# Kernel tuning notes

Measured on AMD Instinct MI355X. Metric: run time of the kernel, lower is better.

Reference implementation:

```python
import jax, jax.numpy as jnp
import numpy as np

NUM_HEADS = 8


def setup_inputs() -> dict:
    key = jax.random.key(0)
    ks = jax.random.split(key, 8)
    b, m, d = 8, 2048, 512
    sc = 1.0 / np.sqrt(d)
    return {
        "x": jax.random.normal(ks[0], (b, m, d), jnp.float32),
        "w_q": jax.random.normal(ks[1], (d, d), jnp.float32) * sc,
        "w_k": jax.random.normal(ks[2], (d, d), jnp.float32) * sc,
        "w_v": jax.random.normal(ks[3], (d, d), jnp.float32) * sc,
        "in_proj_w": jax.random.normal(ks[4], (3 * d, d), jnp.float32) * sc,
        "in_proj_b": jax.random.normal(ks[5], (3 * d,), jnp.float32) * 0.01,
        "out_w": jax.random.normal(ks[6], (d, d), jnp.float32) * sc,
        "out_b": jax.random.normal(ks[7], (d,), jnp.float32) * 0.01,
    }


def _rope_cos_sin(m, d):
    # faithful to source: theta = 10000 ** (-2*(i-1)/d), i = 0..d/2-1
    i = jnp.arange(d // 2, dtype=jnp.float32)
    theta = jnp.power(10000.0, -2.0 * (i - 1.0) / d)
    ang = jnp.arange(m, dtype=jnp.float32)[:, None] * theta  # [m, d/2]
    return jnp.cos(ang), jnp.sin(ang)


def reference(x, w_q, w_k, w_v, in_proj_w, in_proj_b, out_w, out_b):
    b, m, d = x.shape
    h, hd = NUM_HEADS, d // NUM_HEADS
    c, s = _rope_cos_sin(m, d)

    def rot(t):
        # equivalent to t[pos] @ R[pos] with the source's block-rotation matrix
        te = t.reshape(b, m, d // 2, 2)
        e, o = te[..., 0], te[..., 1]
        return jnp.stack([e * c + o * s, -e * s + o * c], axis=-1).reshape(b, m, d)

    q = rot(x @ w_q.T)
    k = rot(x @ w_k.T)
    v = rot(x @ w_v.T)

    # nn.MultiheadAttention's internal in_proj
    wqi, wki, wvi = jnp.split(in_proj_w, 3, axis=0)
    bqi, bki, bvi = jnp.split(in_proj_b, 3, axis=0)
    q = (q @ wqi.T + bqi).reshape(b, m, h, hd)
    k = (k @ wki.T + bki).reshape(b, m, h, hd)
    v = (v @ wvi.T + bvi).reshape(b, m, h, hd)

    scale = 1.0 / jnp.sqrt(jnp.asarray(hd, x.dtype))
    scores = jnp.einsum("bqhd,bkhd->bhqk", q, k) * scale
    causal = jnp.triu(jnp.ones((m, m), bool), k=1)
    scores = jnp.where(causal, jnp.finfo(x.dtype).min, scores)
    attn = jax.nn.softmax(scores, axis=-1)
    ctx = jnp.einsum("bhqk,bkhd->bqhd", attn, v).reshape(b, m, d)
    return ctx @ out_w.T + out_b
```

## Files before the change

kernel.cpp:

```cpp
#include <hip/hip_runtime.h>
#include <hip/hip_bf16.h>

typedef __attribute__((ext_vector_type(8))) short short8;
typedef __attribute__((ext_vector_type(4))) short short4v;
typedef __attribute__((ext_vector_type(4))) float f32x4;

__device__ __forceinline__ float bf2f(unsigned short u) {
    union { unsigned int i; float f; } v; v.i = ((unsigned int)u) << 16; return v.f;
}
__device__ __forceinline__ unsigned short f2bfh(float f) {
    union { __hip_bfloat16 h; unsigned short u; } c;
    c.h = __float2bfloat16(f);
    return c.u;
}

#define GLDS16(g, l) __builtin_amdgcn_global_load_lds( \
    (const __attribute__((address_space(1))) unsigned int*)(g), \
    (__attribute__((address_space(3))) unsigned int*)(l), 16, 0, 0)

__global__ __launch_bounds__(256) void cvt_one(
    const float* __restrict__ in, unsigned short* __restrict__ out, int nchunk)
{
    int i = blockIdx.x * 256 + threadIdx.x;
    if (i >= nchunk) return;
    f32x4 a = *(const f32x4*)&in[(size_t)i * 8];
    f32x4 b = *(const f32x4*)&in[(size_t)i * 8 + 4];
    short8 o;
    o[0] = (short)f2bfh(a[0]); o[1] = (short)f2bfh(a[1]);
    o[2] = (short)f2bfh(a[2]); o[3] = (short)f2bfh(a[3]);
    o[4] = (short)f2bfh(b[0]); o[5] = (short)f2bfh(b[1]);
    o[6] = (short)f2bfh(b[2]); o[7] = (short)f2bfh(b[3]);
    *(short8*)&out[(size_t)i * 8] = o;
}

__global__ __launch_bounds__(256) void cvt_w(
    const float* __restrict__ wq, const float* __restrict__ wk, const float* __restrict__ wv,
    const float* __restrict__ ipw, const float* __restrict__ ow,
    unsigned short* __restrict__ wqb, unsigned short* __restrict__ ipwb,
    unsigned short* __restrict__ owb)
{
    int z = blockIdx.y;
    const float* src;
    unsigned short* dst;
    if (z < 3)      { src = (z == 0 ? wq : z == 1 ? wk : wv); dst = wqb + (size_t)z * 262144; }
    else if (z < 6) { src = ipw + (size_t)(z - 3) * 262144;   dst = ipwb + (size_t)(z - 3) * 262144; }
    else            { src = ow;                                dst = owb; }
    int i = blockIdx.x * 256 + threadIdx.x;
    f32x4 a = *(const f32x4*)&src[(size_t)i * 8];
    f32x4 b = *(const f32x4*)&src[(size_t)i * 8 + 4];
    short8 o;
    o[0] = (short)f2bfh(a[0]); o[1] = (short)f2bfh(a[1]);
    o[2] = (short)f2bfh(a[2]); o[3] = (short)f2bfh(a[3]);
    o[4] = (short)f2bfh(b[0]); o[5] = (short)f2bfh(b[1]);
    o[6] = (short)f2bfh(b[2]); o[7] = (short)f2bfh(b[3]);
    *(short8*)&dst[(size_t)i * 8] = o;
}

__global__ __launch_bounds__(256) void rope_table(float* __restrict__ ct, float* __restrict__ st)
{
    int i = threadIdx.x;
    int pos = blockIdx.x;
    const float THC = -0.05190512648261308f;
    float theta = exp2f(THC * ((float)i - 1.0f));
    float ang = (float)pos * theta;
    float sn, cs;
    sincosf(ang, &sn, &cs);
    ct[pos * 256 + i] = cs;
    st[pos * 256 + i] = sn;
}

__device__ __forceinline__ void gemm_core(
    const unsigned short* __restrict__ A, int lda,
    const unsigned short* __restrict__ B, int K,
    int rowBase, int colBase, int tid, int lane, int wave,
    short* As, short* Bs, f32x4 (&acc)[4][4])
{
    const int wr = wave >> 1, wc = wave & 1;
    const int lo = lane & 15, hi = lane >> 4;
    for (int k0 = 0; k0 < K; k0 += 64) {
        const unsigned short* Ab = A + (size_t)rowBase * lda + k0;
        const unsigned short* Bb = B + (size_t)colBase * K + k0;
        #pragma unroll
        for (int p = 0; p < 4; ++p) {
            int o = p * 256 + tid;
            GLDS16(&Ab[(size_t)(o >> 3) * lda + (o & 7) * 8], &As[o * 8]);
        }
        #pragma unroll
        for (int p = 0; p < 4; ++p) {
            int o = p * 256 + tid;
            GLDS16(&Bb[(size_t)(o >> 3) * K + (o & 7) * 8], &Bs[o * 8]);
        }
        __syncthreads();
        #pragma unroll
        for (int s = 0; s < 2; ++s) {
            short8 a[4], b[4];
            #pragma unroll
            for (int i = 0; i < 4; ++i)
                a[i] = *(const short8*)&As[(wr * 64 + i * 16 + lo) * 64 + s * 32 + hi * 8];
            #pragma unroll
            for (int j = 0; j < 4; ++j)
                b[j] = *(const short8*)&Bs[(wc * 64 + j * 16 + lo) * 64 + s * 32 + hi * 8];
            #pragma unroll
            for (int i = 0; i < 4; ++i)
                #pragma unroll
                for (int j = 0; j < 4; ++j)
                    acc[i][j] = __builtin_amdgcn_mfma_f32_16x16x32_bf16(a[i], b[j], acc[i][j], 0, 0, 0);
        }
        __syncthreads();
    }
}

template<int HAS_BIAS, int OUT>
__global__ __launch_bounds__(256) void gemm_bt(
    const unsigned short* __restrict__ A, int lda, const unsigned short* __restrict__ B,
    const float* __restrict__ bias, void* __restrict__ Cp,
    int M, int N, int K)
{
    __shared__ __align__(16) short As[128 * 64];
    __shared__ __align__(16) short Bs[128 * 64];
    const int tid = threadIdx.x, lane = tid & 63, wave = tid >> 6;
    const int wr = wave >> 1, wc = wave & 1;
    const int lo = lane & 15, hi = lane >> 4;
    const int rowBase = blockIdx.y * 128;
    const int colBase = blockIdx.x * 128;

    f32x4 acc[4][4] = {};
    gemm_core(A, lda, B, K, rowBase, colBase, tid, lane, wave, As, Bs, acc);

    #pragma unroll
    for (int i = 0; i < 4; ++i) {
        int rowA = rowBase + wr * 64 + i * 16 + hi * 4;
        #pragma unroll
        for (int j = 0; j < 4; ++j) {
            int col = colBase + wc * 64 + j * 16 + lo;
            float bv = HAS_BIAS ? bias[col] : 0.0f;
            #pragma unroll
            for (int r = 0; r < 4; ++r) {
                float v = acc[i][j][r] + bv;
                if (OUT == 1) ((float*)Cp)[(size_t)(rowA + r) * N + col] = v;
                else          ((unsigned short*)Cp)[(size_t)(rowA + r) * N + col] = f2bfh(v);
            }
        }
    }
}

__global__ __launch_bounds__(256) void gemm_inproj(
    const unsigned short* __restrict__ T, const unsigned short* __restrict__ ipwb,
    const float* __restrict__ ipb,
    unsigned short* __restrict__ Qb, unsigned short* __restrict__ Kb,
    unsigned short* __restrict__ Vt)
{
    __shared__ __align__(16) short As[128 * 64];
    __shared__ __align__(16) short Bs[128 * 64];
    const int tid = threadIdx.x, lane = tid & 63, wave = tid >> 6;
    const int wr = wave >> 1, wc = wave & 1;
    const int lo = lane & 15, hi = lane >> 4;
    const int rowBase = blockIdx.y * 128;
    const int colBase = blockIdx.x * 128;
    const int z = blockIdx.z;

    const unsigned short* A = T + z * 512;
    const unsigned short* B = ipwb + (size_t)z * 262144;
    const float* bias = ipb + z * 512;

    f32x4 acc[4][4] = {};
    gemm_core(A, 1536, B, 512, rowBase, colBase, tid, lane, wave, As, Bs, acc);

    unsigned short* Crm = (z == 0) ? Qb : Kb;
    #pragma unroll
    for (int i = 0; i < 4; ++i) {
        int rowA = rowBase + wr * 64 + i * 16 + hi * 4;
        #pragma unroll
        for (int j = 0; j < 4; ++j) {
            int col = colBase + wc * 64 + j * 16 + lo;
            float bv = bias[col];
            if (z == 2) {
                short4v sv;
                #pragma unroll
                for (int r = 0; r < 4; ++r) sv[r] = (short)f2bfh(acc[i][j][r] + bv);
                size_t idx = (((size_t)(rowA >> 11) * 8 + (col >> 6)) * 64 + (col & 63)) * 2048
                             + (rowA & 2047);
                *(short4v*)&Vt[idx] = sv;
            } else {
                #pragma unroll
                for (int r = 0; r < 4; ++r)
                    Crm[(size_t)(rowA + r) * 512 + col] = f2bfh(acc[i][j][r] + bv);
            }
        }
    }
}

__global__ __launch_bounds__(192) void rope_kernel(
    unsigned short* __restrict__ T,
    const float* __restrict__ ct, const float* __restrict__ st)
{
    int row = blockIdx.x;
    int c0 = threadIdx.x * 8;
    int pos = row & 2047;
    int i0 = (c0 & 511) >> 1;
    short8 v = *(short8*)&T[(size_t)row * 1536 + c0];
    f32x4 cs = *(const f32x4*)&ct[pos * 256 + i0];
    f32x4 sn = *(const f32x4*)&st[pos * 256 + i0];
    #pragma unroll
    for (int p = 0; p < 4; ++p) {
        float e = bf2f((unsigned short)v[2 * p]);
        float o = bf2f((unsigned short)v[2 * p + 1]);
        v[2 * p]     = (short)f2bfh(e * cs[p] + o * sn[p]);
        v[2 * p + 1] = (short)f2bfh(-e * sn[p] + o * cs[p]);
    }
    *(short8*)&T[(size_t)row * 1536 + c0] = v;
}


__device__ __forceinline__ void attn_step(
    int kt, int NT, int qrow, int lo, int hi,
    const short* __restrict__ KsB, const short* __restrict__ VsB,
    short* __restrict__ Pw,
    short8 (&aq)[2], f32x4 (&o_acc)[4],
    float (&m_i)[4], float (&l_i)[4])
{
    const int swz = (lo & 7) << 3;

    f32x4 sa[4] = {};
    #pragma unroll
    for (int s = 0; s < 2; ++s) {
        short8 bk[4];
        #pragma unroll
        for (int n = 0; n < 4; ++n)
            bk[n] = *(const short8*)&KsB[(n * 16 + lo) * 64 + ((s * 32 + hi * 8) ^ swz)];
        #pragma unroll
        for (int n = 0; n < 4; ++n)
            sa[n] = __builtin_amdgcn_mfma_f32_16x16x32_bf16(aq[s], bk[n], sa[n], 0, 0, 0);
    }

    const bool need_mask = (kt == NT - 1);
    float sv[4][4];
    #pragma unroll
    for (int n = 0; n < 4; ++n) {
        int key = kt * 64 + n * 16 + lo;
        #pragma unroll
        for (int r = 0; r < 4; ++r) {
            float x = sa[n][r];
            if (need_mask) {
                int qr = qrow + hi * 4 + r;
                if (key > qr) x = -1e30f;
            }
            sv[n][r] = x;
        }
    }

    float alpha[4];
    #pragma unroll
    for (int r = 0; r < 4; ++r) {
        float x = fmaxf(fmaxf(sv[0][r], sv[1][r]), fmaxf(sv[2][r], sv[3][r]));
        #pragma unroll
        for (int off = 1; off < 16; off <<= 1) x = fmaxf(x, __shfl_xor(x, off));
        float mn = fmaxf(m_i[r], x);
        alpha[r] = __expf(m_i[r] - mn);
        m_i[r] = mn;
    }
    #pragma unroll
    for (int n = 0; n < 4; ++n)
        #pragma unroll
        for (int r = 0; r < 4; ++r)
            sv[n][r] = __expf(sv[n][r] - m_i[r]);

    #pragma unroll
    for (int r = 0; r < 4; ++r) {
        float x = sv[0][r] + sv[1][r] + sv[2][r] + sv[3][r];
        #pragma unroll
        for (int off = 1; off < 16; off <<= 1) x += __shfl_xor(x, off);
        l_i[r] = l_i[r] * alpha[r] + x;
    }
    #pragma unroll
    for (int t = 0; t < 4; ++t)
        #pragma unroll
        for (int r = 0; r < 4; ++r)
            o_acc[t][r] *= alpha[r];

    #pragma unroll
    for (int n = 0; n < 4; ++n)
        #pragma unroll
        for (int r = 0; r < 4; ++r)
            Pw[(hi * 4 + r) * 72 + n * 16 + lo] = (short)f2bfh(sv[n][r]);

    #pragma unroll
    for (int s = 0; s < 2; ++s) {
        short8 ap = *(const short8*)&Pw[lo * 72 + s * 32 + hi * 8];
        #pragma unroll
        for (int t = 0; t < 4; ++t) {
            short8 bv = *(const short8*)&VsB[(t * 16 + lo) * 64 + ((s * 32 + hi * 8) ^ swz)];
            o_acc[t] = __builtin_amdgcn_mfma_f32_16x16x32_bf16(ap, bv, o_acc[t], 0, 0, 0);
        }
    }
}

#define STG_LOAD(kt, KR0, KR1, VR0, VR1) { \
    int rr = tid >> 3, cc = (tid & 7) * 8; \
    KR0 = *(const short8*)&Kp[(rowQ + (size_t)((kt) * 64 + rr)) * 512 + colBase + cc]; \
    KR1 = *(const short8*)&Kp[(rowQ + (size_t)((kt) * 64 + rr + 32)) * 512 + colBase + cc]; \
    VR0 = *(const short8*)&Vh[(size_t)rr * 2048 + (kt) * 64 + cc]; \
    VR1 = *(const short8*)&Vh[(size_t)(rr + 32) * 2048 + (kt) * 64 + cc]; }

#define STG_WRITE(BUF, KR0, KR1, VR0, VR1) { \
    int rr = tid >> 3; \
    int sw = ((tid & 7) * 8) ^ ((rr & 7) << 3); \
    *(short8*)&Ks[BUF][rr * 64 + sw] = KR0; \
    *(short8*)&Ks[BUF][(rr + 32) * 64 + sw] = KR1; \
    *(short8*)&Vs[BUF][rr * 64 + sw] = VR0; \
    *(short8*)&Vs[BUF][(rr + 32) * 64 + sw] = VR1; }

__global__ __launch_bounds__(256, 3) void attn_kernel(
    const unsigned short* __restrict__ Q, const unsigned short* __restrict__ Kp,
    const unsigned short* __restrict__ Vt, unsigned short* __restrict__ O)
{
    const int tid = threadIdx.x, lane = tid & 63, wave = tid >> 6;
    const int lo = lane & 15, hi = lane >> 4;
    const int bh = blockIdx.x;
    const int qb = 31 - blockIdx.y;
    const int bb = bh >> 3, hh = bh & 7;
    const int NT = qb + 1;

    __shared__ __align__(16) short Ks[2][64 * 64];
    __shared__ __align__(16) short Vs[2][64 * 64];
    __shared__ __align__(16) short P[4][16 * 72];
    short* Pw = P[wave];

    const size_t rowQ = (size_t)bb * 2048;
    const int colBase = hh * 64;
    const unsigned short* Vh = Vt + (size_t)bh * 64 * 2048;
    const int qrow = qb * 64 + wave * 16;

    short8 aq[2];
    #pragma unroll
    for (int s = 0; s < 2; ++s) {
        aq[s] = *(const short8*)&Q[(rowQ + qrow + lo) * 512 + colBase + s * 32 + hi * 8];
        #pragma unroll
        for (int e = 0; e < 8; ++e)
            aq[s][e] = (short)f2bfh(bf2f((unsigned short)aq[s][e]) * 0.125f);
    }

    f32x4 o_acc[4] = {};
    float m_i[4], l_i[4];
    #pragma unroll
    for (int r = 0; r < 4; ++r) { m_i[r] = -1e30f; l_i[r] = 0.0f; }

    short8 ka0, ka1, va0, va1;
    short8 kb0, kb1, vb0, vb1;

    STG_LOAD(0, ka0, ka1, va0, va1);
    STG_WRITE(0, ka0, ka1, va0, va1);
    if (1 < NT) STG_LOAD(1, kb0, kb1, vb0, vb1);
    __syncthreads();

    for (int kt = 0; kt < NT; ) {
        if (kt + 1 < NT) STG_WRITE(1, kb0, kb1, vb0, vb1);
        if (kt + 2 < NT) STG_LOAD(kt + 2, ka0, ka1, va0, va1);
        attn_step(kt, NT, qrow, lo, hi, Ks[0], Vs[0], Pw, aq, o_acc, m_i, l_i);
        __syncthreads();
        ++kt;
        if (kt >= NT) break;
        if (kt + 1 < NT) STG_WRITE(0, ka0, ka1, va0, va1);
        if (kt + 2 < NT) STG_LOAD(kt + 2, kb0, kb1, vb0, vb1);
        attn_step(kt, NT, qrow, lo, hi, Ks[1], Vs[1], Pw, aq, o_acc, m_i, l_i);
        __syncthreads();
        ++kt;
    }

    #pragma unroll
    for (int t = 0; t < 4; ++t)
        #pragma unroll
        for (int r = 0; r < 4; ++r) {
            float v = o_acc[t][r] / l_i[r];
            O[(rowQ + qrow + hi * 4 + r) * 512 + colBase + t * 16 + lo] = f2bfh(v);
        }
}

extern "C" void kernel_launch(void* const* d_in, const int* in_sizes, int n_in,
                              void* d_out, int out_size, void* d_ws, size_t ws_size,
                              hipStream_t stream)
{
    (void)in_sizes; (void)n_in; (void)out_size; (void)ws_size;
    const float* x   = (const float*)d_in[0];
    const float* w_q = (const float*)d_in[1];
    const float* w_k = (const float*)d_in[2];
    const float* w_v = (const float*)d_in[3];
    const float* ipw = (const float*)d_in[4];
    const float* ipb = (const float*)d_in[5];
    const float* ow  = (const float*)d_in[6];
    const float* ob  = (const float*)d_in[7];

    const int M = 16384;
    const size_t SZ = (size_t)M * 512;
    unsigned short* xb   = (unsigned short*)d_ws;
    unsigned short* wqb  = xb + SZ;
    unsigned short* ipwb = wqb + 786432;
    unsigned short* owb  = ipwb + 786432;
    unsigned short* T    = owb + 262144;
    unsigned short* Kb   = T + (size_t)M * 1536;
    unsigned short* Vt   = Kb + SZ;
    float* ct = (float*)(Vt + SZ);
    float* st = ct + 524288;
    unsigned short* Qb   = xb;
    unsigned short* Cb   = T;

    dim3 blk(256);

    cvt_one<<<dim3((int)(SZ / 8 / 256)), blk, 0, stream>>>(x, xb, (int)(SZ / 8));
    cvt_w<<<dim3(128, 7), blk, 0, stream>>>(w_q, w_k, w_v, ipw, ow, wqb, ipwb, owb);
    rope_table<<<dim3(2048), blk, 0, stream>>>(ct, st);

    gemm_bt<0, 0><<<dim3(12, 128), blk, 0, stream>>>(xb, 512, wqb, nullptr, T, M, 1536, 512);

    rope_kernel<<<dim3(M), dim3(192), 0, stream>>>(T, ct, st);

    gemm_inproj<<<dim3(4, 128, 3), blk, 0, stream>>>(T, ipwb, ipb, Qb, Kb, Vt);

    attn_kernel<<<dim3(64, 32), blk, 0, stream>>>(Qb, Kb, Vt, Cb);

    gemm_bt<1, 1><<<dim3(4, 128), blk, 0, stream>>>(Cb, 512, owb, ob, (float*)d_out, M, 512, 512);
}
```

Measured before the change: 338.7 us.

## Fuse RoPE into QKV projection GEMM epilogue and swizzle attention P buffer

The separate rope_kernel pass is removed, and the rotation is applied in the epilogue of the first projection GEMM. Each lane exchanges its even/odd partner with a lane shuffle, and the cos/sin table is transposed to [freq][pos] so each thread reads four consecutive positions as one vector. This drops a full read-modify-write of the 16384x1536 bf16 intermediate and one launch. Separately, the attention kernel's per-wave P scratch changes from a padded stride of 72 to an XOR-swizzled stride of 64, and the occupancy hint rises from 3 to 4 blocks per SIMD, which may add register pressure or spills.

```diff
diff --git a/kernel.cpp b/kernel.cpp
--- a/kernel.cpp
+++ b/kernel.cpp
@@ -58,15 +58,16 @@
 
 __global__ __launch_bounds__(256) void rope_table(float* __restrict__ ct, float* __restrict__ st)
 {
-    int i = threadIdx.x;
-    int pos = blockIdx.x;
+    int i = blockIdx.x;
     const float THC = -0.05190512648261308f;
     float theta = exp2f(THC * ((float)i - 1.0f));
-    float ang = (float)pos * theta;
-    float sn, cs;
-    sincosf(ang, &sn, &cs);
-    ct[pos * 256 + i] = cs;
-    st[pos * 256 + i] = sn;
+    for (int k = 0; k < 8; ++k) {
+        int pos = k * 256 + threadIdx.x;
+        float sn, cs;
+        sincosf((float)pos * theta, &sn, &cs);
+        ct[i * 2048 + pos] = cs;
+        st[i * 2048 + pos] = sn;
+    }
 }
 
 __device__ __forceinline__ void gemm_core(
@@ -139,6 +140,44 @@
                 float v = acc[i][j][r] + bv;
                 if (OUT == 1) ((float*)Cp)[(size_t)(rowA + r) * N + col] = v;
                 else          ((unsigned short*)Cp)[(size_t)(rowA + r) * N + col] = f2bfh(v);
+            }
+        }
+    }
+}
+
+__global__ __launch_bounds__(256) void gemm_rope(
+    const unsigned short* __restrict__ A, const unsigned short* __restrict__ B,
+    unsigned short* __restrict__ T,
+    const float* __restrict__ ct, const float* __restrict__ st)
+{
+    __shared__ __align__(16) short As[128 * 64];
+    __shared__ __align__(16) short Bs[128 * 64];
+    const int tid = threadIdx.x, lane = tid & 63, wave = tid >> 6;
+    const int wr = wave >> 1, wc = wave & 1;
+    const int lo = lane & 15, hi = lane >> 4;
+    const int rowBase = blockIdx.y * 128;
+    const int colBase = blockIdx.x * 128;
+
+    f32x4 acc[4][4] = {};
+    gemm_core(A, 512, B, 512, rowBase, colBase, tid, lane, wave, As, Bs, acc);
+
+    const float sgn = (lane & 1) ? -1.0f : 1.0f;
+    #pragma unroll
+    for (int i = 0; i < 4; ++i) {
+        int rowA = rowBase + wr * 64 + i * 16 + hi * 4;
+        int pos0 = rowA & 2047;
+        #pragma unroll
+        for (int j = 0; j < 4; ++j) {
+            int col = colBase + wc * 64 + j * 16 + lo;
+            int ii = (col & 511) >> 1;
+            f32x4 cs = *(const f32x4*)&ct[ii * 2048 + pos0];
+            f32x4 sn = *(const f32x4*)&st[ii * 2048 + pos0];
+            #pragma unroll
+            for (int r = 0; r < 4; ++r) {
+                float v = acc[i][j][r];
+                float p = __shfl_xor(v, 1);
+                float o = v * cs[r] + sgn * p * sn[r];
+                T[(size_t)(rowA + r) * 1536 + col] = f2bfh(o);
             }
         }
     }
@@ -190,27 +229,6 @@
     }
 }
 
-__global__ __launch_bounds__(192) void rope_kernel(
-    unsigned short* __restrict__ T,
-    const float* __restrict__ ct, const float* __restrict__ st)
-{
-    int row = blockIdx.x;
-    int c0 = threadIdx.x * 8;
-    int pos = row & 2047;
-    int i0 = (c0 & 511) >> 1;
-    short8 v = *(short8*)&T[(size_t)row * 1536 + c0];
-    f32x4 cs = *(const f32x4*)&ct[pos * 256 + i0];
-    f32x4 sn = *(const f32x4*)&st[pos * 256 + i0];
-    #pragma unroll
-    for (int p = 0; p < 4; ++p) {
-        float e = bf2f((unsigned short)v[2 * p]);
-        float o = bf2f((unsigned short)v[2 * p + 1]);
-        v[2 * p]     = (short)f2bfh(e * cs[p] + o * sn[p]);
-        v[2 * p + 1] = (short)f2bfh(-e * sn[p] + o * cs[p]);
-    }
-    *(short8*)&T[(size_t)row * 1536 + c0] = v;
-}
-
 
 __device__ __forceinline__ void attn_step(
     int kt, int NT, int qrow, int lo, int hi,
@@ -281,12 +299,14 @@
     #pragma unroll
     for (int n = 0; n < 4; ++n)
         #pragma unroll
-        for (int r = 0; r < 4; ++r)
-            Pw[(hi * 4 + r) * 72 + n * 16 + lo] = (short)f2bfh(sv[n][r]);
+        for (int r = 0; r < 4; ++r) {
+            int prow = hi * 4 + r;
+            Pw[prow * 64 + ((n * 16 + lo) ^ ((prow & 7) << 3))] = (short)f2bfh(sv[n][r]);
+        }
 
     #pragma unroll
     for (int s = 0; s < 2; ++s) {
-        short8 ap = *(const short8*)&Pw[lo * 72 + s * 32 + hi * 8];
+        short8 ap = *(const short8*)&Pw[lo * 64 + ((s * 32 + hi * 8) ^ swz)];
         #pragma unroll
         for (int t = 0; t < 4; ++t) {
             short8 bv = *(const short8*)&VsB[(t * 16 + lo) * 64 + ((s * 32 + hi * 8) ^ swz)];
@@ -310,7 +330,7 @@
     *(short8*)&Vs[BUF][rr * 64 + sw] = VR0; \
     *(short8*)&Vs[BUF][(rr + 32) * 64 + sw] = VR1; }
 
-__global__ __launch_bounds__(256, 3) void attn_kernel(
+__global__ __launch_bounds__(256, 4) void attn_kernel(
     const unsigned short* __restrict__ Q, const unsigned short* __restrict__ Kp,
     const unsigned short* __restrict__ Vt, unsigned short* __restrict__ O)
 {
@@ -323,7 +343,7 @@
 
     __shared__ __align__(16) short Ks[2][64 * 64];
     __shared__ __align__(16) short Vs[2][64 * 64];
-    __shared__ __align__(16) short P[4][16 * 72];
+    __shared__ __align__(16) short P[4][16 * 64];
     short* Pw = P[wave];
 
     const size_t rowQ = (size_t)bb * 2048;
@@ -408,11 +428,9 @@
 
     cvt_one<<<dim3((int)(SZ / 8 / 256)), blk, 0, stream>>>(x, xb, (int)(SZ / 8));
     cvt_w<<<dim3(128, 7), blk, 0, stream>>>(w_q, w_k, w_v, ipw, ow, wqb, ipwb, owb);
-    rope_table<<<dim3(2048), blk, 0, stream>>>(ct, st);
-
-    gemm_bt<0, 0><<<dim3(12, 128), blk, 0, stream>>>(xb, 512, wqb, nullptr, T, M, 1536, 512);
-
-    rope_kernel<<<dim3(M), dim3(192), 0, stream>>>(T, ct, st);
+    rope_table<<<dim3(256), blk, 0, stream>>>(ct, st);
+
+    gemm_rope<<<dim3(12, 128), blk, 0, stream>>>(xb, wqb, T, ct, st);
 
     gemm_inproj<<<dim3(4, 128, 3), blk, 0, stream>>>(T, ipwb, ipb, Qb, Kb, Vt);
 
```

After: 363.1 us. 1.07x slower.
